# Performance work log

Hardware: AMD Instinct MI355X
Metric: run time of the kernel (lower is better)

The kernel has to match this reference:

```python
import jax, jax.numpy as jnp
import numpy as np

B, S, D, E, K, FF = 4, 2048, 1024, 8, 2, 4096  # batch, seq, d_model, experts, top-k, 4*d_model


def setup_inputs() -> dict:
    key = jax.random.key(0)
    k0, k1, k2, k3 = jax.random.split(key, 4)
    scale = 0.02
    return {
        "x": jax.random.normal(k0, (B, S, D), jnp.float32),
        "gate_w": jax.random.normal(k1, (D, E), jnp.float32) * scale,
        "w1": jax.random.normal(k2, (E, D, FF), jnp.float32) * scale,
        "b1": jnp.zeros((E, FF), jnp.float32),
        "w2": jax.random.normal(k3, (E, FF, D), jnp.float32) * scale,
        "b2": jnp.zeros((E, D), jnp.float32),
    }


def reference(x, gate_w, w1, b1, w2, b2):
    # Gating: top-k logits, softmax over the selected k (matches torch.topk + softmax)
    logits = jnp.einsum("bsd,de->bse", x, gate_w)  # [B,S,E]
    vals, idxs = jax.lax.top_k(logits, K)           # [B,S,K]
    w = jax.nn.softmax(vals, axis=-1)               # [B,S,K]
    n_exp = gate_w.shape[-1]
    # Per-token combine weight for each expert (0 if not selected)
    combine = jnp.sum(jax.nn.one_hot(idxs, n_exp, dtype=x.dtype) * w[..., None], axis=-2)  # [B,S,E]

    out = jnp.zeros_like(x)
    for e in range(n_exp):  # fixed small loop over experts
        h = jax.nn.silu(jnp.einsum("bsd,df->bsf", x, w1[e]) + b1[e])  # dropout = identity (eval)
        y = jnp.einsum("bsf,fd->bsd", h, w2[e]) + b2[e]
        out = out + combine[..., e:e + 1] * y
    return out
```

## Files before the change

### kernel.cpp

```cpp
#include <hip/hip_runtime.h>
#include <math.h>

#define Tt 8192
#define Dd 1024
#define Ee 8
#define FFf 4096
#define SLOTS (Tt*2)

typedef unsigned short u16;
typedef unsigned int u32;
typedef __attribute__((ext_vector_type(8))) __bf16 bf16x8;
typedef __attribute__((ext_vector_type(4))) float f32x4;

__device__ __forceinline__ u16 f2bf(float f) {
  union { float f; u32 u; } v; v.f = f;
  u32 u = v.u;
  return (u16)((u + 0x7FFFu + ((u >> 16) & 1u)) >> 16);
}
__device__ __forceinline__ float bf2f(u16 h) {
  union { u32 u; float f; } v; v.u = ((u32)h) << 16; return v.f;
}
__device__ __forceinline__ void gl2lds16(const u16* g, u16* l) {
  __builtin_amdgcn_global_load_lds((const __attribute__((address_space(1))) void*)g,
                                   (__attribute__((address_space(3))) void*)l, 16, 0, 0);
}

__global__ void gate_topk_kernel(const float* __restrict__ x,
                                 const float* __restrict__ gw,
                                 int* __restrict__ counts,
                                 int* __restrict__ tok_e,
                                 float* __restrict__ tok_w) {
  int wave = (int)((blockIdx.x * blockDim.x + threadIdx.x) >> 6);
  int lane = threadIdx.x & 63;
  if (wave >= Tt) return;
  const float* xrow = x + (size_t)wave * Dd;
  float p[Ee];
#pragma unroll
  for (int e = 0; e < Ee; e++) p[e] = 0.f;
  int d0 = lane * 16;
#pragma unroll
  for (int i = 0; i < 16; i++) {
    float xv = xrow[d0 + i];
    const float* g = gw + (size_t)(d0 + i) * Ee;
#pragma unroll
    for (int e = 0; e < Ee; e++) p[e] += xv * g[e];
  }
#pragma unroll
  for (int e = 0; e < Ee; e++) {
    for (int off = 32; off > 0; off >>= 1) p[e] += __shfl_xor(p[e], off, 64);
  }
  if (lane == 0) {
    int e0 = 0; float v0 = p[0];
#pragma unroll
    for (int e = 1; e < Ee; e++) if (p[e] > v0) { v0 = p[e]; e0 = e; }
    int e1 = -1; float v1 = -INFINITY;
#pragma unroll
    for (int e = 0; e < Ee; e++) if (e != e0 && p[e] > v1) { v1 = p[e]; e1 = e; }
    float w0 = 1.f / (1.f + expf(v1 - v0));
    float w1 = 1.f - w0;
    tok_e[wave * 2 + 0] = e0; tok_e[wave * 2 + 1] = e1;
    tok_w[wave * 2 + 0] = w0; tok_w[wave * 2 + 1] = w1;
    atomicAdd(&counts[e0], 1);
    atomicAdd(&counts[e1], 1);
  }
}

__global__ void xb_convert_kernel(const float* __restrict__ x, u16* __restrict__ xb) {
  int i = blockIdx.x * blockDim.x + threadIdx.x;
  const float* s = x + (size_t)i * 8;
  f32x4 v0 = *(const f32x4*)(s);
  f32x4 v1 = *(const f32x4*)(s + 4);
  uint4 o;
  o.x = (u32)f2bf(v0[0]) | ((u32)f2bf(v0[1]) << 16);
  o.y = (u32)f2bf(v0[2]) | ((u32)f2bf(v0[3]) << 16);
  o.z = (u32)f2bf(v1[0]) | ((u32)f2bf(v1[1]) << 16);
  o.w = (u32)f2bf(v1[2]) | ((u32)f2bf(v1[3]) << 16);
  *(uint4*)(xb + (size_t)i * 8) = o;
}

__global__ __launch_bounds__(256) void wconv_kernel(const float* __restrict__ src,
                                                    u16* __restrict__ dst, int R, int C) {
  __shared__ u16 t[64][72];
  int e = blockIdx.z;
  size_t ebase = (size_t)e * R * C;
  int r0 = blockIdx.y * 64, c0 = blockIdx.x * 64;
  int tid = threadIdx.x;
  int row = tid >> 2, seg = tid & 3;
  const float* sp = src + ebase + (size_t)(r0 + row) * C + c0 + seg * 16;
  f32x4 v0 = *(const f32x4*)(sp);
  f32x4 v1 = *(const f32x4*)(sp + 4);
  f32x4 v2 = *(const f32x4*)(sp + 8);
  f32x4 v3 = *(const f32x4*)(sp + 12);
  uint4 o0, o1;
  o0.x = (u32)f2bf(v0[0]) | ((u32)f2bf(v0[1]) << 16);
  o0.y = (u32)f2bf(v0[2]) | ((u32)f2bf(v0[3]) << 16);
  o0.z = (u32)f2bf(v1[0]) | ((u32)f2bf(v1[1]) << 16);
  o0.w = (u32)f2bf(v1[2]) | ((u32)f2bf(v1[3]) << 16);
  o1.x = (u32)f2bf(v2[0]) | ((u32)f2bf(v2[1]) << 16);
  o1.y = (u32)f2bf(v2[2]) | ((u32)f2bf(v2[3]) << 16);
  o1.z = (u32)f2bf(v3[0]) | ((u32)f2bf(v3[1]) << 16);
  o1.w = (u32)f2bf(v3[2]) | ((u32)f2bf(v3[3]) << 16);
  *(uint4*)&t[row][seg * 16] = o0;
  *(uint4*)&t[row][seg * 16 + 8] = o1;
  __syncthreads();
  u32 w[8];
#pragma unroll
  for (int i = 0; i < 8; i++)
    w[i] = (u32)t[seg * 16 + 2 * i][row] | ((u32)t[seg * 16 + 2 * i + 1][row] << 16);
  u16* dp = dst + ebase + (size_t)(c0 + row) * R + r0 + seg * 16;
  uint4 d0, d1;
  d0.x = w[0]; d0.y = w[1]; d0.z = w[2]; d0.w = w[3];
  d1.x = w[4]; d1.y = w[5]; d1.z = w[6]; d1.w = w[7];
  *(uint4*)dp = d0;
  *(uint4*)(dp + 8) = d1;
}

__global__ void scan_kernel(const int* __restrict__ counts,
                            int* __restrict__ offsets, int* __restrict__ cursors) {
  if (threadIdx.x == 0 && blockIdx.x == 0) {
    int acc = 0;
    for (int e = 0; e < Ee; e++) { offsets[e] = acc; cursors[e] = acc; acc += counts[e]; }
  }
}

__global__ void scatter_kernel(const int* __restrict__ tok_e, const float* __restrict__ tok_w,
                               int* __restrict__ cursors,
                               int* __restrict__ slot_token, float* __restrict__ slot_w,
                               int* __restrict__ tok_slot) {
  int t = blockIdx.x * blockDim.x + threadIdx.x;
  if (t >= Tt) return;
#pragma unroll
  for (int k = 0; k < 2; k++) {
    int e = tok_e[t * 2 + k];
    int pos = atomicAdd(&cursors[e], 1);
    slot_token[pos] = t;
    slot_w[pos] = tok_w[t * 2 + k];
    tok_slot[t * 2 + k] = pos;
  }
}

template<int KDIM, int NDIM, int EPI, int GATHER>
__global__ __launch_bounds__(256) void moe_gemm(
    const u16* __restrict__ A, const u16* __restrict__ BT,
    const float* __restrict__ bias,
    const int* __restrict__ offsets, const int* __restrict__ counts,
    const int* __restrict__ slot_token, const float* __restrict__ slot_w,
    u16* __restrict__ O16, float* __restrict__ Of) {
  int e = blockIdx.z;
  int cnt = counts[e];
  int rb = blockIdx.y;
  if (rb * 128 >= cnt) return;
  int off = offsets[e];
  int n0 = blockIdx.x * 128;

  __shared__ u16 As[128 * 32];
  __shared__ u16 Bs[128 * 32];

  int tid = threadIdx.x;
  int lane = tid & 63, wave = tid >> 6;
  int wm = (wave >> 1) * 64, wn = (wave & 1) * 64;
  int lr = lane & 15, g = lane >> 4;

  int kseg = (lane & 3) * 8;
  const u16* BTe = BT + (size_t)e * NDIM * KDIM;
  const u16* baseA[2]; const u16* baseB[2];
  u16* ldsA[2]; u16* ldsB[2];
#pragma unroll
  for (int q = 0; q < 2; q++) {
    int chunk = wave * 2 + q;
    int row = chunk * 16 + (lane >> 2);
    int slotRow = off + rb * 128 + row;
    int amax = off + cnt - 1;
    if (slotRow > amax) slotRow = amax;
    int arow = GATHER ? slot_token[slotRow] : slotRow;
    baseA[q] = A + (size_t)arow * KDIM + kseg;
    baseB[q] = BTe + (size_t)(n0 + row) * KDIM + kseg;
    ldsA[q] = As + chunk * 512;
    ldsB[q] = Bs + chunk * 512;
  }

  f32x4 acc[4][4];
#pragma unroll
  for (int i = 0; i < 4; i++)
#pragma unroll
    for (int j = 0; j < 4; j++) acc[i][j] = (f32x4)(0.0f);

  for (int k0 = 0; k0 < KDIM; k0 += 32) {
    __syncthreads();
    gl2lds16(baseA[0] + k0, ldsA[0]);
    gl2lds16(baseA[1] + k0, ldsA[1]);
    gl2lds16(baseB[0] + k0, ldsB[0]);
    gl2lds16(baseB[1] + k0, ldsB[1]);
    __syncthreads();
    bf16x8 a[4], b[4];
#pragma unroll
    for (int i = 0; i < 4; i++)
      a[i] = *reinterpret_cast<const bf16x8*>(&As[(wm + i * 16 + lr) * 32 + g * 8]);
#pragma unroll
    for (int j = 0; j < 4; j++)
      b[j] = *reinterpret_cast<const bf16x8*>(&Bs[(wn + j * 16 + lr) * 32 + g * 8]);
#pragma unroll
    for (int i = 0; i < 4; i++)
#pragma unroll
      for (int j = 0; j < 4; j++)
        acc[i][j] = __builtin_amdgcn_mfma_f32_16x16x32_bf16(a[i], b[j], acc[i][j], 0, 0, 0);
  }

  int rlim = cnt - rb * 128;
#pragma unroll
  for (int i = 0; i < 4; i++) {
    int mbase = wm + i * 16 + g * 4;
#pragma unroll
    for (int t = 0; t < 4; t++) {
      int m = mbase + t;
      if (m < rlim) {
        int slot = off + rb * 128 + m;
#pragma unroll
        for (int j = 0; j < 4; j++) {
          int n = n0 + wn + j * 16 + lr;
          float v = acc[i][j][t] + bias[e * NDIM + n];
          if (EPI == 0) {
            float sv = v / (1.f + expf(-v));
            O16[(size_t)slot * NDIM + n] = f2bf(sv);
          } else if (EPI == 1) {
            float wv = v * slot_w[slot];
            O16[(size_t)slot * NDIM + n] = f2bf(wv);
          } else {
            int tok = slot_token[slot];
            atomicAdd(Of + (size_t)tok * NDIM + n, v * slot_w[slot]);
          }
        }
      }
    }
  }
}

__global__ void combine_kernel(const u16* __restrict__ y, const int* __restrict__ tok_slot,
                               float* __restrict__ out) {
  int gid = blockIdx.x * blockDim.x + threadIdx.x;
  int t = gid >> 7;
  int seg = gid & 127;
  int s0 = tok_slot[t * 2 + 0], s1 = tok_slot[t * 2 + 1];
  uint4 a = *(const uint4*)(y + (size_t)s0 * Dd + seg * 8);
  uint4 b = *(const uint4*)(y + (size_t)s1 * Dd + seg * 8);
  f32x4 o0, o1;
  o0[0] = bf2f((u16)a.x) + bf2f((u16)b.x);
  o0[1] = bf2f((u16)(a.x >> 16)) + bf2f((u16)(b.x >> 16));
  o0[2] = bf2f((u16)a.y) + bf2f((u16)b.y);
  o0[3] = bf2f((u16)(a.y >> 16)) + bf2f((u16)(b.y >> 16));
  o1[0] = bf2f((u16)a.z) + bf2f((u16)b.z);
  o1[1] = bf2f((u16)(a.z >> 16)) + bf2f((u16)(b.z >> 16));
  o1[2] = bf2f((u16)a.w) + bf2f((u16)b.w);
  o1[3] = bf2f((u16)(a.w >> 16)) + bf2f((u16)(b.w >> 16));
  float* op = out + (size_t)t * Dd + seg * 8;
  *(f32x4*)op = o0;
  *(f32x4*)(op + 4) = o1;
}

extern "C" void kernel_launch(void* const* d_in, const int* in_sizes, int n_in,
                              void* d_out, int out_size, void* d_ws, size_t ws_size,
                              hipStream_t stream) {
  const float* x  = (const float*)d_in[0];
  const float* gw = (const float*)d_in[1];
  const float* w1 = (const float*)d_in[2];
  const float* b1 = (const float*)d_in[3];
  const float* w2 = (const float*)d_in[4];
  const float* b2 = (const float*)d_in[5];
  float* out = (float*)d_out;

  char* ws = (char*)d_ws;
  size_t off_counts = 0;
  size_t off_offsets = 256;
  size_t off_cursors = 512;
  size_t off_tok_e = 1024;
  size_t off_tok_w     = off_tok_e + (size_t)Tt * 2 * 4;
  size_t off_tok_slot  = off_tok_w + (size_t)Tt * 2 * 4;
  size_t off_slot_token= off_tok_slot + (size_t)Tt * 2 * 4;
  size_t off_slot_w    = off_slot_token + (size_t)SLOTS * 4;
  size_t off_xb        = off_slot_w + (size_t)SLOTS * 4;
  size_t off_h         = off_xb + (size_t)Tt * Dd * 2;
  size_t off_wT        = off_h + (size_t)SLOTS * FFf * 2;
  size_t off_y         = off_wT + (size_t)Ee * Dd * FFf * 2;
  size_t need_atomic   = off_y;
  size_t need_full     = off_y + (size_t)SLOTS * Dd * 2;
  if (ws_size < need_atomic) return;
  int use_combine = (ws_size >= need_full) ? 1 : 0;

  int* counts     = (int*)(ws + off_counts);
  int* offsets    = (int*)(ws + off_offsets);
  int* cursors    = (int*)(ws + off_cursors);
  int* tok_e      = (int*)(ws + off_tok_e);
  float* tok_w    = (float*)(ws + off_tok_w);
  int* tok_slot   = (int*)(ws + off_tok_slot);
  int* slot_token = (int*)(ws + off_slot_token);
  float* slot_w   = (float*)(ws + off_slot_w);
  u16* xb         = (u16*)(ws + off_xb);
  u16* h          = (u16*)(ws + off_h);
  u16* wT         = (u16*)(ws + off_wT);
  u16* y          = (u16*)(ws + off_y);

  hipMemsetAsync(ws, 0, 1024, stream);

  gate_topk_kernel<<<Tt / 4, 256, 0, stream>>>(x, gw, counts, tok_e, tok_w);
  xb_convert_kernel<<<(Tt * Dd / 8) / 256, 256, 0, stream>>>(x, xb);
  scan_kernel<<<1, 64, 0, stream>>>(counts, offsets, cursors);
  scatter_kernel<<<Tt / 256, 256, 0, stream>>>(tok_e, tok_w, cursors, slot_token, slot_w, tok_slot);

  {
    dim3 gc(FFf / 64, Dd / 64, Ee);
    wconv_kernel<<<gc, 256, 0, stream>>>(w1, wT, Dd, FFf);
  }
  {
    dim3 g1(FFf / 128, Tt / 128, Ee);
    moe_gemm<Dd, FFf, 0, 1><<<g1, 256, 0, stream>>>(xb, wT, b1, offsets, counts,
                                                    slot_token, slot_w, h, nullptr);
  }
  {
    dim3 gc(Dd / 64, FFf / 64, Ee);
    wconv_kernel<<<gc, 256, 0, stream>>>(w2, wT, FFf, Dd);
  }
  if (use_combine) {
    dim3 g2(Dd / 128, Tt / 128, Ee);
    moe_gemm<FFf, Dd, 1, 0><<<g2, 256, 0, stream>>>(h, wT, b2, offsets, counts,
                                                    slot_token, slot_w, y, nullptr);
    combine_kernel<<<(Tt * 128) / 256, 256, 0, stream>>>(y, tok_slot, out);
  } else {
    hipMemsetAsync(d_out, 0, (size_t)out_size * sizeof(float), stream);
    dim3 g2(Dd / 128, Tt / 128, Ee);
    moe_gemm<FFf, Dd, 2, 0><<<g2, 256, 0, stream>>>(h, wT, b2, offsets, counts,
                                                    slot_token, slot_w, nullptr, out);
  }
}
```

Measured before the change: 840.6 us.

## Add 256x256 double-buffered pipelined MoE GEMM with swizzled LDS

Introduces a 512-thread GEMM kernel with a 256x256 output tile, double-buffered 64-wide K stages in 128KB of LDS, and explicit waitcnt and barrier scheduling. This overlaps global-to-LDS loads with MFMA work and raises arithmetic intensity in the first expert GEMM. The second GEMM keeps 128x128 tiles but moves to 64-wide K steps with an XOR-swizzled LDS layout to cut bank conflicts and halve the barrier count. The risks are fewer blocks for small experts, wasted work on padded rows in the larger tile, and fragile hand-tuned vmcnt counts.

```diff
diff --git a/kernel.cpp b/kernel.cpp
--- a/kernel.cpp
+++ b/kernel.cpp
@@ -139,13 +139,209 @@
   }
 }
 
+#define MFMA16(H)                                                                 \
+  do {                                                                            \
+    acc[H][0][0] = __builtin_amdgcn_mfma_f32_16x16x32_bf16(a0, b0, acc[H][0][0], 0, 0, 0); \
+    acc[H][0][1] = __builtin_amdgcn_mfma_f32_16x16x32_bf16(a0, b1, acc[H][0][1], 0, 0, 0); \
+    acc[H][0][2] = __builtin_amdgcn_mfma_f32_16x16x32_bf16(a0, b2, acc[H][0][2], 0, 0, 0); \
+    acc[H][0][3] = __builtin_amdgcn_mfma_f32_16x16x32_bf16(a0, b3, acc[H][0][3], 0, 0, 0); \
+    acc[H][1][0] = __builtin_amdgcn_mfma_f32_16x16x32_bf16(a1, b0, acc[H][1][0], 0, 0, 0); \
+    acc[H][1][1] = __builtin_amdgcn_mfma_f32_16x16x32_bf16(a1, b1, acc[H][1][1], 0, 0, 0); \
+    acc[H][1][2] = __builtin_amdgcn_mfma_f32_16x16x32_bf16(a1, b2, acc[H][1][2], 0, 0, 0); \
+    acc[H][1][3] = __builtin_amdgcn_mfma_f32_16x16x32_bf16(a1, b3, acc[H][1][3], 0, 0, 0); \
+    acc[H][2][0] = __builtin_amdgcn_mfma_f32_16x16x32_bf16(a2, b0, acc[H][2][0], 0, 0, 0); \
+    acc[H][2][1] = __builtin_amdgcn_mfma_f32_16x16x32_bf16(a2, b1, acc[H][2][1], 0, 0, 0); \
+    acc[H][2][2] = __builtin_amdgcn_mfma_f32_16x16x32_bf16(a2, b2, acc[H][2][2], 0, 0, 0); \
+    acc[H][2][3] = __builtin_amdgcn_mfma_f32_16x16x32_bf16(a2, b3, acc[H][2][3], 0, 0, 0); \
+    acc[H][3][0] = __builtin_amdgcn_mfma_f32_16x16x32_bf16(a3, b0, acc[H][3][0], 0, 0, 0); \
+    acc[H][3][1] = __builtin_amdgcn_mfma_f32_16x16x32_bf16(a3, b1, acc[H][3][1], 0, 0, 0); \
+    acc[H][3][2] = __builtin_amdgcn_mfma_f32_16x16x32_bf16(a3, b2, acc[H][3][2], 0, 0, 0); \
+    acc[H][3][3] = __builtin_amdgcn_mfma_f32_16x16x32_bf16(a3, b3, acc[H][3][3], 0, 0, 0); \
+  } while (0)
+
 template<int KDIM, int NDIM, int EPI, int GATHER>
-__global__ __launch_bounds__(256) void moe_gemm(
+__global__ __launch_bounds__(512, 2) void moe_gemm_big(
     const u16* __restrict__ A, const u16* __restrict__ BT,
     const float* __restrict__ bias,
     const int* __restrict__ offsets, const int* __restrict__ counts,
     const int* __restrict__ slot_token, const float* __restrict__ slot_w,
     u16* __restrict__ O16, float* __restrict__ Of) {
+  constexpr int NT = KDIM / 64;
+  int e = blockIdx.z;
+  int cnt = counts[e];
+  int rb = blockIdx.y;
+  if (rb * 256 >= cnt) return;
+  int off = offsets[e];
+  int n0 = blockIdx.x * 256;
+
+  __shared__ u16 S[65536];
+
+  int tid = threadIdx.x;
+  int lane = tid & 63, wave = tid >> 6;
+  int wr = wave >> 2, wc = wave & 3;
+  int lr = lane & 15, g = lane >> 4;
+
+  const u16* BTe = BT + (size_t)e * NDIM * KDIM;
+
+  const u16* aSrc[2][2];
+  const u16* bSrc[2][2];
+  int amax = off + cnt - 1;
+#pragma unroll
+  for (int h = 0; h < 2; h++)
+#pragma unroll
+    for (int s = 0; s < 2; s++) {
+      int c = tid + s * 512;
+      int lc = c ^ (((c >> 5) & 1) << 1);
+      int ks = lc >> 9, rl = (lc >> 2) & 127, seg = lc & 3;
+      int slotRow = off + rb * 256 + h * 128 + rl;
+      if (slotRow > amax) slotRow = amax;
+      int arow = GATHER ? slot_token[slotRow] : slotRow;
+      aSrc[h][s] = A + (size_t)arow * KDIM + ks * 32 + seg * 8;
+    }
+#pragma unroll
+  for (int ks = 0; ks < 2; ks++)
+#pragma unroll
+    for (int s = 0; s < 2; s++) {
+      int c = tid + s * 512;
+      int lc = c ^ (((c >> 5) & 1) << 1);
+      int row = lc >> 2, seg = lc & 3;
+      bSrc[ks][s] = BTe + (size_t)(n0 + row) * KDIM + ks * 32 + seg * 8;
+    }
+
+  auto stA = [&](int u, int h) {
+    u16* d = &S[(u & 1) * 16384 + h * 8192 + wave * 512];
+    gl2lds16(aSrc[h][0] + (size_t)u * 64, d);
+    gl2lds16(aSrc[h][1] + (size_t)u * 64, d + 4096);
+  };
+  auto stB = [&](int u, int ks) {
+    u16* d = &S[32768 + (u & 1) * 16384 + ks * 8192 + wave * 512];
+    gl2lds16(bSrc[ks][0] + (size_t)u * 64, d);
+    gl2lds16(bSrc[ks][1] + (size_t)u * 64, d + 4096);
+  };
+  auto rdA = [&](int dbuf, int hm, int ks, int i) -> bf16x8 {
+    int rl = wr * 64 + i * 16 + lr;
+    int logb = ks * 8192 + rl * 64 + g * 16;
+    int phys = logb ^ (((rl >> 3) & 1) << 5);
+    return *reinterpret_cast<const bf16x8*>(&S[dbuf * 16384 + hm * 8192 + (phys >> 1)]);
+  };
+  auto rdB = [&](int dbuf, int ks, int j) -> bf16x8 {
+    int row = wc * 64 + j * 16 + lr;
+    int logb = row * 64 + g * 16;
+    int phys = logb ^ (((row >> 3) & 1) << 5);
+    return *reinterpret_cast<const bf16x8*>(&S[32768 + dbuf * 16384 + ks * 8192 + (phys >> 1)]);
+  };
+
+  f32x4 acc[2][4][4];
+#pragma unroll
+  for (int h = 0; h < 2; h++)
+#pragma unroll
+    for (int i = 0; i < 4; i++)
+#pragma unroll
+      for (int j = 0; j < 4; j++) acc[h][i][j] = (f32x4)(0.0f);
+
+  stB(0, 0); stA(0, 0); stA(0, 1); stB(0, 1);
+  stB(1, 0); stA(1, 0);
+  asm volatile("s_waitcnt vmcnt(4)" ::: "memory");
+  __builtin_amdgcn_s_barrier();
+
+  bf16x8 b0, b1, b2, b3;
+  for (int t = 0; t < NT; ++t) {
+    int dbuf = t & 1;
+    {
+      bf16x8 a0 = rdA(dbuf, 0, 0, 0), a1 = rdA(dbuf, 0, 0, 1),
+             a2 = rdA(dbuf, 0, 0, 2), a3 = rdA(dbuf, 0, 0, 3);
+      b0 = rdB(dbuf, 0, 0); b1 = rdB(dbuf, 0, 1); b2 = rdB(dbuf, 0, 2); b3 = rdB(dbuf, 0, 3);
+      if (t + 1 < NT) stA(t + 1, 1);
+      __builtin_amdgcn_s_barrier();
+      asm volatile("s_waitcnt lgkmcnt(0)" ::: "memory");
+      __builtin_amdgcn_sched_barrier(0);
+      __builtin_amdgcn_s_setprio(1);
+      MFMA16(0);
+      __builtin_amdgcn_s_setprio(0);
+      __builtin_amdgcn_s_barrier();
+    }
+    {
+      bf16x8 a0 = rdA(dbuf, 1, 0, 0), a1 = rdA(dbuf, 1, 0, 1),
+             a2 = rdA(dbuf, 1, 0, 2), a3 = rdA(dbuf, 1, 0, 3);
+      if (t + 1 < NT) {
+        stB(t + 1, 1);
+        asm volatile("s_waitcnt vmcnt(8)" ::: "memory");
+      }
+      __builtin_amdgcn_s_barrier();
+      asm volatile("s_waitcnt lgkmcnt(0)" ::: "memory");
+      __builtin_amdgcn_sched_barrier(0);
+      __builtin_amdgcn_s_setprio(1);
+      MFMA16(1);
+      __builtin_amdgcn_s_setprio(0);
+      __builtin_amdgcn_s_barrier();
+    }
+    {
+      bf16x8 a0 = rdA(dbuf, 0, 1, 0), a1 = rdA(dbuf, 0, 1, 1),
+             a2 = rdA(dbuf, 0, 1, 2), a3 = rdA(dbuf, 0, 1, 3);
+      b0 = rdB(dbuf, 1, 0); b1 = rdB(dbuf, 1, 1); b2 = rdB(dbuf, 1, 2); b3 = rdB(dbuf, 1, 3);
+      if (t + 2 < NT) stB(t + 2, 0);
+      __builtin_amdgcn_s_barrier();
+      asm volatile("s_waitcnt lgkmcnt(0)" ::: "memory");
+      __builtin_amdgcn_sched_barrier(0);
+      __builtin_amdgcn_s_setprio(1);
+      MFMA16(0);
+      __builtin_amdgcn_s_setprio(0);
+      __builtin_amdgcn_s_barrier();
+    }
+    {
+      bf16x8 a0 = rdA(dbuf, 1, 1, 0), a1 = rdA(dbuf, 1, 1, 1),
+             a2 = rdA(dbuf, 1, 1, 2), a3 = rdA(dbuf, 1, 1, 3);
+      if (t + 2 < NT) {
+        stA(t + 2, 0);
+        asm volatile("s_waitcnt vmcnt(6)" ::: "memory");
+      } else if (t + 1 < NT) {
+        asm volatile("s_waitcnt vmcnt(0)" ::: "memory");
+      }
+      __builtin_amdgcn_s_barrier();
+      asm volatile("s_waitcnt lgkmcnt(0)" ::: "memory");
+      __builtin_amdgcn_sched_barrier(0);
+      __builtin_amdgcn_s_setprio(1);
+      MFMA16(1);
+      __builtin_amdgcn_s_setprio(0);
+      __builtin_amdgcn_s_barrier();
+    }
+  }
+
+  int rlim = cnt - rb * 256;
+#pragma unroll
+  for (int hm = 0; hm < 2; hm++)
+#pragma unroll
+    for (int i = 0; i < 4; i++)
+#pragma unroll
+      for (int q = 0; q < 4; q++) {
+        int m = hm * 128 + wr * 64 + i * 16 + g * 4 + q;
+        if (m < rlim) {
+          int slot = off + rb * 256 + m;
+#pragma unroll
+          for (int j = 0; j < 4; j++) {
+            int n = n0 + wc * 64 + j * 16 + lr;
+            float v = acc[hm][i][j][q] + bias[e * NDIM + n];
+            if (EPI == 0) {
+              float sv = v / (1.f + expf(-v));
+              O16[(size_t)slot * NDIM + n] = f2bf(sv);
+            } else if (EPI == 1) {
+              O16[(size_t)slot * NDIM + n] = f2bf(v * slot_w[slot]);
+            } else {
+              atomicAdd(Of + (size_t)slot_token[slot] * NDIM + n, v * slot_w[slot]);
+            }
+          }
+        }
+      }
+}
+
+template<int KDIM, int NDIM, int EPI, int GATHER>
+__global__ __launch_bounds__(256) void moe_gemm_sm(
+    const u16* __restrict__ A, const u16* __restrict__ BT,
+    const float* __restrict__ bias,
+    const int* __restrict__ offsets, const int* __restrict__ counts,
+    const int* __restrict__ slot_token, const float* __restrict__ slot_w,
+    u16* __restrict__ O16, float* __restrict__ Of) {
+  constexpr int NT = KDIM / 64;
   int e = blockIdx.z;
   int cnt = counts[e];
   int rb = blockIdx.y;
@@ -153,30 +349,27 @@
   int off = offsets[e];
   int n0 = blockIdx.x * 128;
 
-  __shared__ u16 As[128 * 32];
-  __shared__ u16 Bs[128 * 32];
+  __shared__ u16 S[16384];
 
   int tid = threadIdx.x;
   int lane = tid & 63, wave = tid >> 6;
   int wm = (wave >> 1) * 64, wn = (wave & 1) * 64;
   int lr = lane & 15, g = lane >> 4;
 
-  int kseg = (lane & 3) * 8;
   const u16* BTe = BT + (size_t)e * NDIM * KDIM;
-  const u16* baseA[2]; const u16* baseB[2];
-  u16* ldsA[2]; u16* ldsB[2];
-#pragma unroll
-  for (int q = 0; q < 2; q++) {
-    int chunk = wave * 2 + q;
-    int row = chunk * 16 + (lane >> 2);
-    int slotRow = off + rb * 128 + row;
-    int amax = off + cnt - 1;
+  const u16* aS[4];
+  const u16* bS[4];
+  int amax = off + cnt - 1;
+#pragma unroll
+  for (int s = 0; s < 4; s++) {
+    int c = tid + s * 256;
+    int lc = c ^ (((c >> 5) & 1) << 1);
+    int ks = lc >> 9, rl = (lc >> 2) & 127, seg = lc & 3;
+    int slotRow = off + rb * 128 + rl;
     if (slotRow > amax) slotRow = amax;
     int arow = GATHER ? slot_token[slotRow] : slotRow;
-    baseA[q] = A + (size_t)arow * KDIM + kseg;
-    baseB[q] = BTe + (size_t)(n0 + row) * KDIM + kseg;
-    ldsA[q] = As + chunk * 512;
-    ldsB[q] = Bs + chunk * 512;
+    aS[s] = A + (size_t)arow * KDIM + ks * 32 + seg * 8;
+    bS[s] = BTe + (size_t)(n0 + rl) * KDIM + ks * 32 + seg * 8;
   }
 
   f32x4 acc[4][4];
@@ -185,54 +378,63 @@
 #pragma unroll
     for (int j = 0; j < 4; j++) acc[i][j] = (f32x4)(0.0f);
 
-  for (int k0 = 0; k0 < KDIM; k0 += 32) {
+  for (int t = 0; t < NT; ++t) {
     __syncthreads();
-    gl2lds16(baseA[0] + k0, ldsA[0]);
-    gl2lds16(baseA[1] + k0, ldsA[1]);
-    gl2lds16(baseB[0] + k0, ldsB[0]);
-    gl2lds16(baseB[1] + k0, ldsB[1]);
+#pragma unroll
+    for (int s = 0; s < 4; s++)
+      gl2lds16(aS[s] + (size_t)t * 64, &S[s * 2048 + wave * 512]);
+#pragma unroll
+    for (int s = 0; s < 4; s++)
+      gl2lds16(bS[s] + (size_t)t * 64, &S[8192 + s * 2048 + wave * 512]);
     __syncthreads();
-    bf16x8 a[4], b[4];
-#pragma unroll
-    for (int i = 0; i < 4; i++)
-      a[i] = *reinterpret_cast<const bf16x8*>(&As[(wm + i * 16 + lr) * 32 + g * 8]);
-#pragma unroll
-    for (int j = 0; j < 4; j++)
-      b[j] = *reinterpret_cast<const bf16x8*>(&Bs[(wn + j * 16 + lr) * 32 + g * 8]);
-#pragma unroll
-    for (int i = 0; i < 4; i++)
-#pragma unroll
-      for (int j = 0; j < 4; j++)
-        acc[i][j] = __builtin_amdgcn_mfma_f32_16x16x32_bf16(a[i], b[j], acc[i][j], 0, 0, 0);
+#pragma unroll
+    for (int ks = 0; ks < 2; ks++) {
+      bf16x8 a[4], b[4];
+#pragma unroll
+      for (int i = 0; i < 4; i++) {
+        int rl = wm + i * 16 + lr;
+        int logb = ks * 8192 + rl * 64 + g * 16;
+        int phys = logb ^ (((rl >> 3) & 1) << 5);
+        a[i] = *reinterpret_cast<const bf16x8*>(&S[phys >> 1]);
+      }
+#pragma unroll
+      for (int j = 0; j < 4; j++) {
+        int row = wn + j * 16 + lr;
+        int logb = ks * 8192 + row * 64 + g * 16;
+        int phys = logb ^ (((row >> 3) & 1) << 5);
+        b[j] = *reinterpret_cast<const bf16x8*>(&S[8192 + (phys >> 1)]);
+      }
+#pragma unroll
+      for (int i = 0; i < 4; i++)
+#pragma unroll
+        for (int j = 0; j < 4; j++)
+          acc[i][j] = __builtin_amdgcn_mfma_f32_16x16x32_bf16(a[i], b[j], acc[i][j], 0, 0, 0);
+    }
   }
 
   int rlim = cnt - rb * 128;
 #pragma unroll
-  for (int i = 0; i < 4; i++) {
-    int mbase = wm + i * 16 + g * 4;
-#pragma unroll
-    for (int t = 0; t < 4; t++) {
-      int m = mbase + t;
+  for (int i = 0; i < 4; i++)
+#pragma unroll
+    for (int q = 0; q < 4; q++) {
+      int m = wm + i * 16 + g * 4 + q;
       if (m < rlim) {
         int slot = off + rb * 128 + m;
 #pragma unroll
         for (int j = 0; j < 4; j++) {
           int n = n0 + wn + j * 16 + lr;
-          float v = acc[i][j][t] + bias[e * NDIM + n];
+          float v = acc[i][j][q] + bias[e * NDIM + n];
           if (EPI == 0) {
             float sv = v / (1.f + expf(-v));
             O16[(size_t)slot * NDIM + n] = f2bf(sv);
           } else if (EPI == 1) {
-            float wv = v * slot_w[slot];
-            O16[(size_t)slot * NDIM + n] = f2bf(wv);
+            O16[(size_t)slot * NDIM + n] = f2bf(v * slot_w[slot]);
           } else {
-            int tok = slot_token[slot];
-            atomicAdd(Of + (size_t)tok * NDIM + n, v * slot_w[slot]);
+            atomicAdd(Of + (size_t)slot_token[slot] * NDIM + n, v * slot_w[slot]);
           }
         }
       }
     }
-  }
 }
 
 __global__ void combine_kernel(const u16* __restrict__ y, const int* __restrict__ tok_slot,
@@ -311,9 +513,9 @@
     wconv_kernel<<<gc, 256, 0, stream>>>(w1, wT, Dd, FFf);
   }
   {
-    dim3 g1(FFf / 128, Tt / 128, Ee);
-    moe_gemm<Dd, FFf, 0, 1><<<g1, 256, 0, stream>>>(xb, wT, b1, offsets, counts,
-                                                    slot_token, slot_w, h, nullptr);
+    dim3 g1(FFf / 256, Tt / 256, Ee);
+    moe_gemm_big<Dd, FFf, 0, 1><<<g1, 512, 0, stream>>>(xb, wT, b1, offsets, counts,
+                                                        slot_token, slot_w, h, nullptr);
   }
   {
     dim3 gc(Dd / 64, FFf / 64, Ee);
@@ -321,13 +523,13 @@
   }
   if (use_combine) {
     dim3 g2(Dd / 128, Tt / 128, Ee);
-    moe_gemm<FFf, Dd, 1, 0><<<g2, 256, 0, stream>>>(h, wT, b2, offsets, counts,
-                                                    slot_token, slot_w, y, nullptr);
+    moe_gemm_sm<FFf, Dd, 1, 0><<<g2, 256, 0, stream>>>(h, wT, b2, offsets, counts,
+                                                       slot_token, slot_w, y, nullptr);
     combine_kernel<<<(Tt * 128) / 256, 256, 0, stream>>>(y, tok_slot, out);
   } else {
     hipMemsetAsync(d_out, 0, (size_t)out_size * sizeof(float), stream);
     dim3 g2(Dd / 128, Tt / 128, Ee);
-    moe_gemm<FFf, Dd, 2, 0><<<g2, 256, 0, stream>>>(h, wT, b2, offsets, counts,
-                                                    slot_token, slot_w, nullptr, out);
-  }
-}
+    moe_gemm_sm<FFf, Dd, 2, 0><<<g2, 256, 0, stream>>>(h, wT, b2, offsets, counts,
+                                                       slot_token, slot_w, nullptr, out);
+  }
+}
```

New measurement: 847.0 us. No clear change (+0.8%).
